# Optimization experiments

Measured on AMD Instinct MI355X. Metric: run time of the kernel, lower is better.

## Reference

```python
import jax, jax.numpy as jnp
import numpy as np

EPS = 1e-5
DIL = 2
PAD = 2  # dilation * (kernel_size - 1) // 2


def _conv(x, w, dil, pad):
    return jax.lax.conv_general_dilated(
        x, w, window_strides=(1, 1), padding=[(pad, pad), (pad, pad)],
        rhs_dilation=(dil, dil), dimension_numbers=('NCHW', 'OIHW', 'NCHW'))


def _bn(x, g, b):
    # BatchNorm2d in training mode: per-channel batch stats over (N,H,W)
    m = x.mean(axis=(0, 2, 3), keepdims=True)
    v = x.var(axis=(0, 2, 3), keepdims=True)
    return (x - m) * jax.lax.rsqrt(v + EPS) * g[None, :, None, None] + b[None, :, None, None]


def _deform_conv(x, offset, w, dil=DIL, pad=PAD):
    # torchvision deform_conv2d v1 (no modulation): offset [B, 2*K, H, W] with
    # channel ordering (dy_0, dx_0, dy_1, dx_1, ...), kernel tap k = ky*3 + kx.
    B, C, H, W = x.shape
    Co = w.shape[0]
    K = 9
    off = offset.reshape(B, K, 2, H, W)
    dy, dx = off[:, :, 0], off[:, :, 1]              # [B,K,H,W]
    kr = jnp.arange(3)
    kyy = (jnp.repeat(kr, 3) * dil - pad).astype(x.dtype)   # [K]
    kxx = (jnp.tile(kr, 3) * dil - pad).astype(x.dtype)     # [K]
    hg = jnp.arange(H, dtype=x.dtype)
    wg = jnp.arange(W, dtype=x.dtype)
    py = hg[None, None, :, None] + kyy[None, :, None, None] + dy   # [B,K,H,W]
    px = wg[None, None, None, :] + kxx[None, :, None, None] + dx   # [B,K,H,W]
    y0 = jnp.floor(py)
    x0 = jnp.floor(px)
    wy = py - y0   # [B,K,H,W]
    wx = px - x0
    y0i = y0.astype(jnp.int32)
    x0i = x0.astype(jnp.int32)
    x_flat = x.reshape(B, C, H * W)

    def corner(yi, xi):
        valid = ((yi >= 0) & (yi < H) & (xi >= 0) & (xi < W)).astype(x.dtype)  # [B,K,H,W]
        idx = jnp.clip(yi, 0, H - 1) * W + jnp.clip(xi, 0, W - 1)
        v = jax.vmap(lambda xb, ib: xb[:, ib])(x_flat, idx.reshape(B, -1))    # [B,C,K*H*W]
        return v.reshape(B, C, K, H, W) * valid[:, None]

    v00 = corner(y0i, x0i)
    v01 = corner(y0i, x0i + 1)
    v10 = corner(y0i + 1, x0i)
    v11 = corner(y0i + 1, x0i + 1)
    wy_ = wy[:, None]   # [B,1,K,H,W]
    wx_ = wx[:, None]
    sampled = (v00 * (1 - wy_) * (1 - wx_) + v01 * (1 - wy_) * wx_
               + v10 * wy_ * (1 - wx_) + v11 * wy_ * wx_)          # [B,C,K,H,W]
    return jnp.einsum('bckhw,ock->bohw', sampled, w.reshape(Co, C, K))


def setup_inputs() -> dict:
    key = jax.random.key(0)
    ks = jax.random.split(key, 4)
    B, C, H, W = 4, 256, 56, 56
    x = jax.random.normal(ks[0], (B, C, H, W), dtype=jnp.float32)
    w_off = jax.random.normal(ks[1], (18, C, 3, 3), dtype=jnp.float32) * 0.01
    b_off = jnp.zeros((18,), dtype=jnp.float32)
    w1 = jax.random.normal(ks[2], (C, C, 3, 3), dtype=jnp.float32) * (1.0 / np.sqrt(9 * C))
    w2 = jax.random.normal(ks[3], (C, C, 3, 3), dtype=jnp.float32) * (1.0 / np.sqrt(9 * C))
    gamma1 = jnp.ones((C,), dtype=jnp.float32)
    beta1 = jnp.zeros((C,), dtype=jnp.float32)
    gamma2 = jnp.ones((C,), dtype=jnp.float32)
    beta2 = jnp.zeros((C,), dtype=jnp.float32)
    return {'x': x, 'w_off': w_off, 'b_off': b_off, 'w1': w1, 'gamma1': gamma1,
            'beta1': beta1, 'w2': w2, 'gamma2': gamma2, 'beta2': beta2}


def reference(x, w_off, b_off, w1, gamma1, beta1, w2, gamma2, beta2):
    offset = _conv(x, w_off, DIL, PAD) + b_off[None, :, None, None]   # [B,18,H,W]
    out = _deform_conv(x, offset, w1)
    out = jax.nn.relu(_bn(out, gamma1, beta1))
    out = _conv(out, w2, 1, 1)
    out = _bn(out, gamma2, beta2)
    return jax.nn.relu(out + x)
```

## Files before the change

kernel.cpp:

```cpp
#include <hip/hip_runtime.h>

typedef __bf16 bf16;
typedef bf16 bf16x4 __attribute__((ext_vector_type(4)));
typedef bf16 bf16x8 __attribute__((ext_vector_type(8)));
typedef float f32x4 __attribute__((ext_vector_type(4)));

#define CH 256
#define HH 56
#define WW 56
#define HW 3136
#define MM 12544
#define KT 2304

__device__ __forceinline__ void gll16(const bf16* g, bf16* l) {
  __builtin_amdgcn_global_load_lds(
      (const __attribute__((address_space(1))) void*)g,
      (__attribute__((address_space(3))) void*)l, 16, 0, 0);
}

__global__ __launch_bounds__(256) void nchw2nhwc_k(const float* __restrict__ x,
                                                   bf16* __restrict__ o) {
  __shared__ float t[32][33];
  const int b = blockIdx.z, hw0 = blockIdx.x * 32, c0 = blockIdx.y * 32;
  const int tid = threadIdx.x;
  {
    const int cl = tid >> 3, hwl = (tid & 7) * 4;
    f32x4 v = *(const f32x4*)&x[(size_t)(b * CH + c0 + cl) * HW + hw0 + hwl];
#pragma unroll
    for (int i = 0; i < 4; ++i) t[cl][hwl + i] = v[i];
  }
  __syncthreads();
  const int hwl = tid >> 3, cl = (tid & 7) * 4;
  bf16x4 ov;
#pragma unroll
  for (int i = 0; i < 4; ++i) ov[i] = (bf16)t[cl + i][hwl];
  *(bf16x4*)&o[(size_t)(b * HW + hw0 + hwl) * CH + c0 + cl] = ov;
}

__global__ void reorder_w_k(const float* __restrict__ in, bf16* __restrict__ out,
                            int Nsrc, int Ntot) {
  const int idx = blockIdx.x * 256 + threadIdx.x;
  if (idx >= Ntot * KT) return;
  const int o = idx / KT, r = idx - o * KT;
  const int k = r >> 8, c = r & 255;
  float v = (o < Nsrc) ? in[(size_t)(o * CH + c) * 9 + k] : 0.f;
  out[idx] = (bf16)v;
}

__global__ __launch_bounds__(256) void build_deform_k(
    const bf16* __restrict__ xn, const float* __restrict__ offb,
    const float* __restrict__ boff, bf16* __restrict__ A1) {
  const int tid = threadIdx.x;
  const int m = blockIdx.x * 32 + (tid >> 3);
  const int l7 = tid & 7;
  const int b = m / HW, hw = m - b * HW;
  const int h = hw / WW, w = hw - h * WW;
  const float* orow = offb + m * 18;
  const bf16* xb = xn + (size_t)b * HW * CH;
  bf16* dst = A1 + (size_t)m * KT;
  for (int tap = 0; tap < 9; ++tap) {
    const int ky = tap / 3, kx = tap - ky * 3;
    const float dy = orow[2 * tap] + boff[2 * tap];
    const float dx = orow[2 * tap + 1] + boff[2 * tap + 1];
    const float py = (float)(h + ky * 2 - 2) + dy;
    const float px = (float)(w + kx * 2 - 2) + dx;
    const float y0f = floorf(py), x0f = floorf(px);
    const int y0 = (int)y0f, x0 = (int)x0f;
    const float wy = py - y0f, wx = px - x0f;
    const float w00 = (1.f - wy) * (1.f - wx), w01 = (1.f - wy) * wx;
    const float w10 = wy * (1.f - wx), w11 = wy * wx;
    const bool vy0 = (unsigned)y0 < HH, vy1 = (unsigned)(y0 + 1) < HH;
    const bool vx0 = (unsigned)x0 < WW, vx1 = (unsigned)(x0 + 1) < WW;
    const bf16* p00 = xb + (long long)(y0 * WW + x0) * CH;
#pragma unroll
    for (int j = 0; j < 4; ++j) {
      const int cc = j * 64 + l7 * 8;
      bf16x8 v00 = {}, v01 = {}, v10 = {}, v11 = {};
      if (vy0 && vx0) v00 = *(const bf16x8*)(p00 + cc);
      if (vy0 && vx1) v01 = *(const bf16x8*)(p00 + CH + cc);
      if (vy1 && vx0) v10 = *(const bf16x8*)(p00 + WW * CH + cc);
      if (vy1 && vx1) v11 = *(const bf16x8*)(p00 + WW * CH + CH + cc);
      bf16x8 o;
#pragma unroll
      for (int i = 0; i < 8; ++i)
        o[i] = (bf16)(w00 * (float)v00[i] + w01 * (float)v01[i] +
                      w10 * (float)v10[i] + w11 * (float)v11[i]);
      *(bf16x8*)(dst + tap * 256 + cc) = o;
    }
  }
}

template <int MODE, int EPI, int SWZ>
__global__ __launch_bounds__(256, 3) void gemm_k(
    const bf16* __restrict__ Asrc, const bf16* __restrict__ Bt,
    const bf16* __restrict__ zp, bf16* __restrict__ outb,
    float* __restrict__ sS, float* __restrict__ sQ,
    float* __restrict__ offout, const int ksteps, const int dil, const int pad) {
  __shared__ __align__(16) bf16 Ab[2][4096];
  __shared__ __align__(16) bf16 Bb[2][4096];
  const int tid = threadIdx.x;
  int n0, m0;
  if (SWZ) {
    const int gid = blockIdx.x;
    const int swz = (gid & 7) * 98 + (gid >> 3);
    n0 = (swz & 3) * 64;
    m0 = (swz >> 2) * 64;
  } else {
    n0 = blockIdx.x * 64;
    m0 = blockIdx.y * 64;
  }
  const int kbase = blockIdx.z * ksteps * 64;
  const int lane = tid & 63, wv = tid >> 6;
  const int wrM = wv >> 1, wcN = wv & 1;
  const int fr = lane & 15, kg = lane >> 4;
  const int srow = tid >> 3, cpos = tid & 7;
  const int sxor = (cpos ^ (srow & 7)) * 8;

  int bb[2], hh[2], wwv[2];
  const bf16* aptr[2];
  if (MODE == 1) {
#pragma unroll
    for (int pa = 0; pa < 2; ++pa) {
      const int m = m0 + pa * 32 + srow;
      bb[pa] = m / HW;
      const int hw = m - bb[pa] * HW;
      hh[pa] = hw / WW;
      wwv[pa] = hw - hh[pa] * WW;
    }
  } else {
#pragma unroll
    for (int pa = 0; pa < 2; ++pa)
      aptr[pa] = Asrc + (size_t)(m0 + pa * 32 + srow) * KT + kbase + sxor;
  }
  const bf16* bptr[2];
#pragma unroll
  for (int pb = 0; pb < 2; ++pb)
    bptr[pb] = Bt + (size_t)(n0 + pb * 32 + srow) * KT + kbase + sxor;

  f32x4 acc[2][2] = {};

  auto STAGE = [&](int kt, int buf) {
    const int kk = kbase + kt * 64;
#pragma unroll
    for (int pa = 0; pa < 2; ++pa) {
      const bf16* as;
      if (MODE == 0) {
        as = aptr[pa] + kt * 64;
      } else {
        const int tap = kk >> 8, coff = kk & 255;
        const int ky = tap / 3, kx = tap - ky * 3;
        const int y = hh[pa] + ky * dil - pad, xx = wwv[pa] + kx * dil - pad;
        const bool ok = ((unsigned)y < HH) && ((unsigned)xx < WW);
        as = ok ? Asrc + ((size_t)(bb[pa] * HW + y * WW + xx) * CH + coff + sxor)
                : zp + sxor;
      }
      gll16(as, &Ab[buf][(pa * 32 + srow) * 64 + cpos * 8]);
    }
#pragma unroll
    for (int pb = 0; pb < 2; ++pb)
      gll16(bptr[pb] + kt * 64, &Bb[buf][(pb * 32 + srow) * 64 + cpos * 8]);
  };

  auto COMPUTE = [&](int buf) {
#pragma unroll
    for (int kh = 0; kh < 2; ++kh) {
      bf16x8 af[2], bv[2];
#pragma unroll
      for (int mf = 0; mf < 2; ++mf) {
        const int row = wrM * 32 + mf * 16 + fr;
        const int g = (kh * 4 + kg) ^ (row & 7);
        af[mf] = *(const bf16x8*)&Ab[buf][row * 64 + g * 8];
      }
#pragma unroll
      for (int nf = 0; nf < 2; ++nf) {
        const int row = wcN * 32 + nf * 16 + fr;
        const int g = (kh * 4 + kg) ^ (row & 7);
        bv[nf] = *(const bf16x8*)&Bb[buf][row * 64 + g * 8];
      }
#pragma unroll
      for (int mf = 0; mf < 2; ++mf)
#pragma unroll
        for (int nf = 0; nf < 2; ++nf)
          acc[mf][nf] = __builtin_amdgcn_mfma_f32_16x16x32_bf16(af[mf], bv[nf],
                                                                acc[mf][nf], 0, 0, 0);
    }
  };

  STAGE(0, 0);
  STAGE(1, 1);
  int buf = 0;
  for (int kt = 0; kt < ksteps; ++kt) {
    if (kt + 1 < ksteps) {
      asm volatile("s_waitcnt vmcnt(4)" ::: "memory");
    } else {
      asm volatile("s_waitcnt vmcnt(0)" ::: "memory");
    }
    __builtin_amdgcn_s_barrier();
    __builtin_amdgcn_sched_barrier(0);
    COMPUTE(buf);
    __builtin_amdgcn_sched_barrier(0);
    __builtin_amdgcn_s_barrier();
    if (kt + 2 < ksteps) STAGE(kt + 2, buf);
    buf ^= 1;
  }

  if (EPI == 1) {
#pragma unroll
    for (int mf = 0; mf < 2; ++mf) {
      const int rr = m0 + wrM * 32 + mf * 16 + kg * 4;
#pragma unroll
      for (int nf = 0; nf < 2; ++nf) {
        const int col = n0 + wcN * 32 + nf * 16 + fr;
#pragma unroll
        for (int r = 0; r < 4; ++r)
          outb[(size_t)(rr + r) * CH + col] = (bf16)acc[mf][nf][r];
      }
    }
    float ps[2], pq[2];
#pragma unroll
    for (int nf = 0; nf < 2; ++nf) {
      float s = 0.f, q = 0.f;
#pragma unroll
      for (int mf = 0; mf < 2; ++mf)
#pragma unroll
        for (int r = 0; r < 4; ++r) {
          const float v = acc[mf][nf][r];
          s += v;
          q += v * v;
        }
      s += __shfl_xor(s, 16);
      s += __shfl_xor(s, 32);
      q += __shfl_xor(q, 16);
      q += __shfl_xor(q, 32);
      ps[nf] = s;
      pq[nf] = q;
    }
    float* red = (float*)&Ab[0][0];
    if (tid < 128) red[tid] = 0.f;
    __syncthreads();
    if (kg == 0) {
#pragma unroll
      for (int nf = 0; nf < 2; ++nf) {
        const int cb = wcN * 32 + nf * 16 + fr;
        atomicAdd(&red[cb], ps[nf]);
        atomicAdd(&red[64 + cb], pq[nf]);
      }
    }
    __syncthreads();
    if (tid < 64) {
      atomicAdd(&sS[n0 + tid], red[tid]);
      atomicAdd(&sQ[n0 + tid], red[64 + tid]);
    }
  } else {
#pragma unroll
    for (int mf = 0; mf < 2; ++mf) {
      const int rr = m0 + wrM * 32 + mf * 16 + kg * 4;
#pragma unroll
      for (int nf = 0; nf < 2; ++nf) {
        const int col = n0 + wcN * 32 + nf * 16 + fr;
        if (col < 18) {
#pragma unroll
          for (int r = 0; r < 4; ++r)
            atomicAdd(&offout[(size_t)(rr + r) * 18 + col], acc[mf][nf][r]);
        }
      }
    }
  }
}

__global__ void affine_k(const float* __restrict__ s, const float* __restrict__ sq,
                         const float* __restrict__ g, const float* __restrict__ be,
                         float* __restrict__ sc, float* __restrict__ bi) {
  const int c = threadIdx.x;
  const float inv = 1.f / (float)MM;
  const float mean = s[c] * inv;
  const float var = sq[c] * inv - mean * mean;
  const float scale = g[c] * rsqrtf(var + 1e-5f);
  sc[c] = scale;
  bi[c] = be[c] - mean * scale;
}

__global__ __launch_bounds__(256) void a1_kb(const bf16* __restrict__ in,
                                             const float* __restrict__ sc,
                                             const float* __restrict__ bi,
                                             bf16* __restrict__ out) {
  const size_t idx = (size_t)(blockIdx.x * 256 + threadIdx.x) * 8;
  const int c0 = (int)(idx & 255);
  bf16x8 v = *(const bf16x8*)&in[idx];
  bf16x8 o;
#pragma unroll
  for (int i = 0; i < 8; ++i) {
    float r = (float)v[i] * sc[c0 + i] + bi[c0 + i];
    o[i] = (bf16)(r > 0.f ? r : 0.f);
  }
  *(bf16x8*)&out[idx] = o;
}

__global__ __launch_bounds__(256) void final_kb(const bf16* __restrict__ o2,
                                                const float* __restrict__ x,
                                                const float* __restrict__ sc,
                                                const float* __restrict__ bi,
                                                float* __restrict__ out) {
  __shared__ float t[32][33];
  const int b = blockIdx.z, hw0 = blockIdx.x * 32, o0 = blockIdx.y * 32;
  const int tid = threadIdx.x;
  {
    const int hwl = tid >> 3, ol = (tid & 7) * 4;
    bf16x4 v = *(const bf16x4*)&o2[(size_t)(b * HW + hw0 + hwl) * CH + o0 + ol];
#pragma unroll
    for (int i = 0; i < 4; ++i) t[ol + i][hwl] = (float)v[i];
  }
  __syncthreads();
  const int ol = tid >> 3, hwl = (tid & 7) * 4;
  const int ch = o0 + ol;
  const float s = sc[ch], bb = bi[ch];
  const size_t xi = (size_t)(b * CH + ch) * HW + hw0 + hwl;
  f32x4 xv = *(const f32x4*)&x[xi];
  f32x4 r;
#pragma unroll
  for (int i = 0; i < 4; ++i) {
    float v = t[ol][hwl + i] * s + bb + xv[i];
    r[i] = v > 0.f ? v : 0.f;
  }
  *(f32x4*)&out[xi] = r;
}

#define WS_XN 0ULL
#define WS_W1T 6422528ULL
#define WS_W2T 7602176ULL
#define WS_WOF 8781824ULL
#define WS_OFFB 9076736ULL
#define WS_A1 9979904ULL
#define WS_O1 67782656ULL
#define WS_ACT 74205184ULL
#define WS_O2 80627712ULL
#define WS_ZP 87050240ULL
#define WS_STAT 87054336ULL
#define WS_SCB 87058432ULL

extern "C" void kernel_launch(void* const* d_in, const int* in_sizes, int n_in,
                              void* d_out, int out_size, void* d_ws, size_t ws_size,
                              hipStream_t stream) {
  const float* x = (const float*)d_in[0];
  const float* w_off = (const float*)d_in[1];
  const float* b_off = (const float*)d_in[2];
  const float* w1 = (const float*)d_in[3];
  const float* g1 = (const float*)d_in[4];
  const float* be1 = (const float*)d_in[5];
  const float* w2 = (const float*)d_in[6];
  const float* g2 = (const float*)d_in[7];
  const float* be2 = (const float*)d_in[8];
  float* out = (float*)d_out;
  char* ws = (char*)d_ws;

  bf16* xn = (bf16*)(ws + WS_XN);
  bf16* w1t = (bf16*)(ws + WS_W1T);
  bf16* w2t = (bf16*)(ws + WS_W2T);
  bf16* wof = (bf16*)(ws + WS_WOF);
  float* offb = (float*)(ws + WS_OFFB);
  bf16* A1 = (bf16*)(ws + WS_A1);
  bf16* o1 = (bf16*)(ws + WS_O1);
  bf16* act = (bf16*)(ws + WS_ACT);
  bf16* o2 = (bf16*)(ws + WS_O2);
  bf16* zp = (bf16*)(ws + WS_ZP);
  float* s1 = (float*)(ws + WS_STAT);
  float* sq1 = (float*)(ws + WS_STAT + 1024);
  float* s2 = (float*)(ws + WS_STAT + 2048);
  float* sq2 = (float*)(ws + WS_STAT + 3072);
  float* sc1 = (float*)(ws + WS_SCB);
  float* bi1 = (float*)(ws + WS_SCB + 1024);
  float* sc2 = (float*)(ws + WS_SCB + 2048);
  float* bi2 = (float*)(ws + WS_SCB + 3072);

  hipMemsetAsync(ws + WS_ZP, 0, 8192, stream);
  hipMemsetAsync(ws + WS_OFFB, 0, 903168, stream);

  nchw2nhwc_k<<<dim3(98, 8, 4), 256, 0, stream>>>(x, xn);
  reorder_w_k<<<2304, 256, 0, stream>>>(w1, w1t, 256, 256);
  reorder_w_k<<<2304, 256, 0, stream>>>(w2, w2t, 256, 256);
  reorder_w_k<<<576, 256, 0, stream>>>(w_off, wof, 18, 64);

  gemm_k<1, 0, 0><<<dim3(1, 196, 4), 256, 0, stream>>>(
      xn, wof, zp, nullptr, nullptr, nullptr, offb, 9, 2, 2);

  build_deform_k<<<392, 256, 0, stream>>>(xn, offb, b_off, A1);

  gemm_k<0, 1, 1><<<dim3(784), 256, 0, stream>>>(A1, w1t, zp, o1, s1, sq1,
                                                 nullptr, 36, 0, 0);
  affine_k<<<1, 256, 0, stream>>>(s1, sq1, g1, be1, sc1, bi1);
  a1_kb<<<1568, 256, 0, stream>>>(o1, sc1, bi1, act);

  gemm_k<1, 1, 1><<<dim3(784), 256, 0, stream>>>(act, w2t, zp, o2, s2, sq2,
                                                 nullptr, 36, 1, 1);
  affine_k<<<1, 256, 0, stream>>>(s2, sq2, g2, be2, sc2, bi2);

  final_kb<<<dim3(98, 8, 4), 256, 0, stream>>>(o2, x, sc2, bi2, out);
}
```

Baseline: 215.9 us.

## Triple-buffer GEMM, merge weight reorders, fold BN affine into consumers

The GEMM kernel moves from double to triple buffering of its LDS stages, and the K-step count and N-tile become template parameters. With TN=32, the offset-conv GEMM loads only 32 weight rows instead of 64. The three weight-reorder launches become one kernel, and the two affine_k launches are removed by computing BN scale and bias inside a1_kb and final_kb. build_deform_k now uses 16 threads per pixel across twice as many blocks. The extra LDS buffer raises shared memory use and could lower occupancy under launch_bounds(256,3), and the fused kernels recompute the BN statistics for every element.

```diff
diff --git a/kernel.cpp b/kernel.cpp
--- a/kernel.cpp
+++ b/kernel.cpp
@@ -16,6 +16,15 @@
   __builtin_amdgcn_global_load_lds(
       (const __attribute__((address_space(1))) void*)g,
       (__attribute__((address_space(3))) void*)l, 16, 0, 0);
+}
+
+template <int N>
+__device__ __forceinline__ void waitvm() {
+  if constexpr (N == 0) asm volatile("s_waitcnt vmcnt(0)" ::: "memory");
+  else if constexpr (N == 3) asm volatile("s_waitcnt vmcnt(3)" ::: "memory");
+  else if constexpr (N == 4) asm volatile("s_waitcnt vmcnt(4)" ::: "memory");
+  else if constexpr (N == 6) asm volatile("s_waitcnt vmcnt(6)" ::: "memory");
+  else if constexpr (N == 8) asm volatile("s_waitcnt vmcnt(8)" ::: "memory");
 }
 
 __global__ __launch_bounds__(256) void nchw2nhwc_k(const float* __restrict__ x,
@@ -37,22 +46,34 @@
   *(bf16x4*)&o[(size_t)(b * HW + hw0 + hwl) * CH + c0 + cl] = ov;
 }
 
-__global__ void reorder_w_k(const float* __restrict__ in, bf16* __restrict__ out,
-                            int Nsrc, int Ntot) {
-  const int idx = blockIdx.x * 256 + threadIdx.x;
-  if (idx >= Ntot * KT) return;
-  const int o = idx / KT, r = idx - o * KT;
-  const int k = r >> 8, c = r & 255;
-  float v = (o < Nsrc) ? in[(size_t)(o * CH + c) * 9 + k] : 0.f;
-  out[idx] = (bf16)v;
+__global__ void reorder_all_k(const float* __restrict__ w1,
+                              const float* __restrict__ w2,
+                              const float* __restrict__ woff,
+                              bf16* __restrict__ w1t, bf16* __restrict__ w2t,
+                              bf16* __restrict__ wof) {
+  const int gid = blockIdx.x;
+  if (gid < 4608) {
+    const int idx = gid * 256 + threadIdx.x;
+    const float* in = (gid < 2304) ? w1 : w2;
+    bf16* out = (gid < 2304) ? w1t : w2t;
+    const int li = (gid < 2304) ? idx : idx - 2304 * 256;
+    const int o = li / KT, r = li - o * KT;
+    const int k = r >> 8, c = r & 255;
+    out[li] = (bf16)in[(size_t)(o * CH + c) * 9 + k];
+  } else {
+    const int li = (gid - 4608) * 256 + threadIdx.x;
+    const int o = li / KT, r = li - o * KT;
+    const int k = r >> 8, c = r & 255;
+    wof[li] = (bf16)((o < 18) ? woff[(size_t)(o * CH + c) * 9 + k] : 0.f);
+  }
 }
 
 __global__ __launch_bounds__(256) void build_deform_k(
     const bf16* __restrict__ xn, const float* __restrict__ offb,
     const float* __restrict__ boff, bf16* __restrict__ A1) {
   const int tid = threadIdx.x;
-  const int m = blockIdx.x * 32 + (tid >> 3);
-  const int l7 = tid & 7;
+  const int m = blockIdx.x * 16 + (tid >> 4);
+  const int l15 = tid & 15;
   const int b = m / HW, hw = m - b * HW;
   const int h = hw / WW, w = hw - h * WW;
   const float* orow = offb + m * 18;
@@ -73,8 +94,8 @@
     const bool vx0 = (unsigned)x0 < WW, vx1 = (unsigned)(x0 + 1) < WW;
     const bf16* p00 = xb + (long long)(y0 * WW + x0) * CH;
 #pragma unroll
-    for (int j = 0; j < 4; ++j) {
-      const int cc = j * 64 + l7 * 8;
+    for (int j = 0; j < 2; ++j) {
+      const int cc = j * 128 + l15 * 8;
       bf16x8 v00 = {}, v01 = {}, v10 = {}, v11 = {};
       if (vy0 && vx0) v00 = *(const bf16x8*)(p00 + cc);
       if (vy0 && vx1) v01 = *(const bf16x8*)(p00 + CH + cc);
@@ -90,14 +111,17 @@
   }
 }
 
-template <int MODE, int EPI, int SWZ>
+template <int MODE, int EPI, int SWZ, int TN, int KS>
 __global__ __launch_bounds__(256, 3) void gemm_k(
     const bf16* __restrict__ Asrc, const bf16* __restrict__ Bt,
     const bf16* __restrict__ zp, bf16* __restrict__ outb,
     float* __restrict__ sS, float* __restrict__ sQ,
-    float* __restrict__ offout, const int ksteps, const int dil, const int pad) {
-  __shared__ __align__(16) bf16 Ab[2][4096];
-  __shared__ __align__(16) bf16 Bb[2][4096];
+    float* __restrict__ offout, const int dil, const int pad) {
+  constexpr int PB = TN / 32;
+  constexpr int NF = TN / 32;
+  constexpr int SL = 2 + PB;
+  __shared__ __align__(16) bf16 Ab[3][4096];
+  __shared__ __align__(16) bf16 Bb[3][TN * 64];
   const int tid = threadIdx.x;
   int n0, m0;
   if (SWZ) {
@@ -106,10 +130,10 @@
     n0 = (swz & 3) * 64;
     m0 = (swz >> 2) * 64;
   } else {
-    n0 = blockIdx.x * 64;
+    n0 = blockIdx.x * TN;
     m0 = blockIdx.y * 64;
   }
-  const int kbase = blockIdx.z * ksteps * 64;
+  const int kbase = blockIdx.z * KS * 64;
   const int lane = tid & 63, wv = tid >> 6;
   const int wrM = wv >> 1, wcN = wv & 1;
   const int fr = lane & 15, kg = lane >> 4;
@@ -132,12 +156,12 @@
     for (int pa = 0; pa < 2; ++pa)
       aptr[pa] = Asrc + (size_t)(m0 + pa * 32 + srow) * KT + kbase + sxor;
   }
-  const bf16* bptr[2];
-#pragma unroll
-  for (int pb = 0; pb < 2; ++pb)
+  const bf16* bptr[PB];
+#pragma unroll
+  for (int pb = 0; pb < PB; ++pb)
     bptr[pb] = Bt + (size_t)(n0 + pb * 32 + srow) * KT + kbase + sxor;
 
-  f32x4 acc[2][2] = {};
+  f32x4 acc[2][NF] = {};
 
   auto STAGE = [&](int kt, int buf) {
     const int kk = kbase + kt * 64;
@@ -157,14 +181,14 @@
       gll16(as, &Ab[buf][(pa * 32 + srow) * 64 + cpos * 8]);
     }
 #pragma unroll
-    for (int pb = 0; pb < 2; ++pb)
+    for (int pb = 0; pb < PB; ++pb)
       gll16(bptr[pb] + kt * 64, &Bb[buf][(pb * 32 + srow) * 64 + cpos * 8]);
   };
 
   auto COMPUTE = [&](int buf) {
 #pragma unroll
     for (int kh = 0; kh < 2; ++kh) {
-      bf16x8 af[2], bv[2];
+      bf16x8 af[2], bv[NF];
 #pragma unroll
       for (int mf = 0; mf < 2; ++mf) {
         const int row = wrM * 32 + mf * 16 + fr;
@@ -172,15 +196,15 @@
         af[mf] = *(const bf16x8*)&Ab[buf][row * 64 + g * 8];
       }
 #pragma unroll
-      for (int nf = 0; nf < 2; ++nf) {
-        const int row = wcN * 32 + nf * 16 + fr;
+      for (int nf = 0; nf < NF; ++nf) {
+        const int row = wcN * (NF * 16) + nf * 16 + fr;
         const int g = (kh * 4 + kg) ^ (row & 7);
         bv[nf] = *(const bf16x8*)&Bb[buf][row * 64 + g * 8];
       }
 #pragma unroll
       for (int mf = 0; mf < 2; ++mf)
 #pragma unroll
-        for (int nf = 0; nf < 2; ++nf)
+        for (int nf = 0; nf < NF; ++nf)
           acc[mf][nf] = __builtin_amdgcn_mfma_f32_16x16x32_bf16(af[mf], bv[nf],
                                                                 acc[mf][nf], 0, 0, 0);
     }
@@ -188,37 +212,36 @@
 
   STAGE(0, 0);
   STAGE(1, 1);
-  int buf = 0;
-  for (int kt = 0; kt < ksteps; ++kt) {
-    if (kt + 1 < ksteps) {
-      asm volatile("s_waitcnt vmcnt(4)" ::: "memory");
-    } else {
-      asm volatile("s_waitcnt vmcnt(0)" ::: "memory");
-    }
+  STAGE(2, 2);
+#pragma unroll 3
+  for (int kt = 0; kt < KS; ++kt) {
+    const int buf = kt % 3;
+    if (kt < KS - 2) waitvm<2 * SL>();
+    else if (kt == KS - 2) waitvm<SL>();
+    else waitvm<0>();
     __builtin_amdgcn_s_barrier();
     __builtin_amdgcn_sched_barrier(0);
     COMPUTE(buf);
     __builtin_amdgcn_sched_barrier(0);
     __builtin_amdgcn_s_barrier();
-    if (kt + 2 < ksteps) STAGE(kt + 2, buf);
-    buf ^= 1;
-  }
-
-  if (EPI == 1) {
+    if (kt + 3 < KS) STAGE(kt + 3, buf);
+  }
+
+  if constexpr (EPI == 1) {
 #pragma unroll
     for (int mf = 0; mf < 2; ++mf) {
       const int rr = m0 + wrM * 32 + mf * 16 + kg * 4;
 #pragma unroll
-      for (int nf = 0; nf < 2; ++nf) {
-        const int col = n0 + wcN * 32 + nf * 16 + fr;
+      for (int nf = 0; nf < NF; ++nf) {
+        const int col = n0 + wcN * (NF * 16) + nf * 16 + fr;
 #pragma unroll
         for (int r = 0; r < 4; ++r)
           outb[(size_t)(rr + r) * CH + col] = (bf16)acc[mf][nf][r];
       }
     }
-    float ps[2], pq[2];
-#pragma unroll
-    for (int nf = 0; nf < 2; ++nf) {
+    float ps[NF], pq[NF];
+#pragma unroll
+    for (int nf = 0; nf < NF; ++nf) {
       float s = 0.f, q = 0.f;
 #pragma unroll
       for (int mf = 0; mf < 2; ++mf)
@@ -240,8 +263,8 @@
     __syncthreads();
     if (kg == 0) {
 #pragma unroll
-      for (int nf = 0; nf < 2; ++nf) {
-        const int cb = wcN * 32 + nf * 16 + fr;
+      for (int nf = 0; nf < NF; ++nf) {
+        const int cb = wcN * (NF * 16) + nf * 16 + fr;
         atomicAdd(&red[cb], ps[nf]);
         atomicAdd(&red[64 + cb], pq[nf]);
       }
@@ -256,8 +279,8 @@
     for (int mf = 0; mf < 2; ++mf) {
       const int rr = m0 + wrM * 32 + mf * 16 + kg * 4;
 #pragma unroll
-      for (int nf = 0; nf < 2; ++nf) {
-        const int col = n0 + wcN * 32 + nf * 16 + fr;
+      for (int nf = 0; nf < NF; ++nf) {
+        const int col = n0 + wcN * (NF * 16) + nf * 16 + fr;
         if (col < 18) {
 #pragma unroll
           for (int r = 0; r < 4; ++r)
@@ -268,29 +291,25 @@
   }
 }
 
-__global__ void affine_k(const float* __restrict__ s, const float* __restrict__ sq,
-                         const float* __restrict__ g, const float* __restrict__ be,
-                         float* __restrict__ sc, float* __restrict__ bi) {
-  const int c = threadIdx.x;
-  const float inv = 1.f / (float)MM;
-  const float mean = s[c] * inv;
-  const float var = sq[c] * inv - mean * mean;
-  const float scale = g[c] * rsqrtf(var + 1e-5f);
-  sc[c] = scale;
-  bi[c] = be[c] - mean * scale;
-}
-
 __global__ __launch_bounds__(256) void a1_kb(const bf16* __restrict__ in,
-                                             const float* __restrict__ sc,
-                                             const float* __restrict__ bi,
+                                             const float* __restrict__ s,
+                                             const float* __restrict__ sq,
+                                             const float* __restrict__ g,
+                                             const float* __restrict__ be,
                                              bf16* __restrict__ out) {
   const size_t idx = (size_t)(blockIdx.x * 256 + threadIdx.x) * 8;
   const int c0 = (int)(idx & 255);
+  const float inv = 1.f / (float)MM;
   bf16x8 v = *(const bf16x8*)&in[idx];
   bf16x8 o;
 #pragma unroll
   for (int i = 0; i < 8; ++i) {
-    float r = (float)v[i] * sc[c0 + i] + bi[c0 + i];
+    const int c = c0 + i;
+    const float mean = s[c] * inv;
+    const float var = sq[c] * inv - mean * mean;
+    const float sc = g[c] * rsqrtf(var + 1e-5f);
+    const float bi = be[c] - mean * sc;
+    float r = (float)v[i] * sc + bi;
     o[i] = (bf16)(r > 0.f ? r : 0.f);
   }
   *(bf16x8*)&out[idx] = o;
@@ -298,8 +317,10 @@
 
 __global__ __launch_bounds__(256) void final_kb(const bf16* __restrict__ o2,
                                                 const float* __restrict__ x,
-                                                const float* __restrict__ sc,
-                                                const float* __restrict__ bi,
+                                                const float* __restrict__ s,
+                                                const float* __restrict__ sq,
+                                                const float* __restrict__ g,
+                                                const float* __restrict__ be,
                                                 float* __restrict__ out) {
   __shared__ float t[32][33];
   const int b = blockIdx.z, hw0 = blockIdx.x * 32, o0 = blockIdx.y * 32;
@@ -313,13 +334,17 @@
   __syncthreads();
   const int ol = tid >> 3, hwl = (tid & 7) * 4;
   const int ch = o0 + ol;
-  const float s = sc[ch], bb = bi[ch];
+  const float inv = 1.f / (float)MM;
+  const float mean = s[ch] * inv;
+  const float var = sq[ch] * inv - mean * mean;
+  const float sc = g[ch] * rsqrtf(var + 1e-5f);
+  const float bb = be[ch] - mean * sc;
   const size_t xi = (size_t)(b * CH + ch) * HW + hw0 + hwl;
   f32x4 xv = *(const f32x4*)&x[xi];
   f32x4 r;
 #pragma unroll
   for (int i = 0; i < 4; ++i) {
-    float v = t[ol][hwl + i] * s + bb + xv[i];
+    float v = t[ol][hwl + i] * sc + bb + xv[i];
     r[i] = v > 0.f ? v : 0.f;
   }
   *(f32x4*)&out[xi] = r;
@@ -336,7 +361,6 @@
 #define WS_O2 80627712ULL
 #define WS_ZP 87050240ULL
 #define WS_STAT 87054336ULL
-#define WS_SCB 87058432ULL
 
 extern "C" void kernel_launch(void* const* d_in, const int* in_sizes, int n_in,
                               void* d_out, int out_size, void* d_ws, size_t ws_size,
@@ -367,32 +391,24 @@
   float* sq1 = (float*)(ws + WS_STAT + 1024);
   float* s2 = (float*)(ws + WS_STAT + 2048);
   float* sq2 = (float*)(ws + WS_STAT + 3072);
-  float* sc1 = (float*)(ws + WS_SCB);
-  float* bi1 = (float*)(ws + WS_SCB + 1024);
-  float* sc2 = (float*)(ws + WS_SCB + 2048);
-  float* bi2 = (float*)(ws + WS_SCB + 3072);
 
   hipMemsetAsync(ws + WS_ZP, 0, 8192, stream);
   hipMemsetAsync(ws + WS_OFFB, 0, 903168, stream);
 
   nchw2nhwc_k<<<dim3(98, 8, 4), 256, 0, stream>>>(x, xn);
-  reorder_w_k<<<2304, 256, 0, stream>>>(w1, w1t, 256, 256);
-  reorder_w_k<<<2304, 256, 0, stream>>>(w2, w2t, 256, 256);
-  reorder_w_k<<<576, 256, 0, stream>>>(w_off, wof, 18, 64);
-
-  gemm_k<1, 0, 0><<<dim3(1, 196, 4), 256, 0, stream>>>(
-      xn, wof, zp, nullptr, nullptr, nullptr, offb, 9, 2, 2);
-
-  build_deform_k<<<392, 256, 0, stream>>>(xn, offb, b_off, A1);
-
-  gemm_k<0, 1, 1><<<dim3(784), 256, 0, stream>>>(A1, w1t, zp, o1, s1, sq1,
-                                                 nullptr, 36, 0, 0);
-  affine_k<<<1, 256, 0, stream>>>(s1, sq1, g1, be1, sc1, bi1);
-  a1_kb<<<1568, 256, 0, stream>>>(o1, sc1, bi1, act);
-
-  gemm_k<1, 1, 1><<<dim3(784), 256, 0, stream>>>(act, w2t, zp, o2, s2, sq2,
-                                                 nullptr, 36, 1, 1);
-  affine_k<<<1, 256, 0, stream>>>(s2, sq2, g2, be2, sc2, bi2);
-
-  final_kb<<<dim3(98, 8, 4), 256, 0, stream>>>(o2, x, sc2, bi2, out);
-}
+  reorder_all_k<<<5184, 256, 0, stream>>>(w1, w2, w_off, w1t, w2t, wof);
+
+  gemm_k<1, 0, 0, 32, 9><<<dim3(1, 196, 4), 256, 0, stream>>>(
+      xn, wof, zp, nullptr, nullptr, nullptr, offb, 2, 2);
+
+  build_deform_k<<<784, 256, 0, stream>>>(xn, offb, b_off, A1);
+
+  gemm_k<0, 1, 1, 64, 36><<<dim3(784), 256, 0, stream>>>(
+      A1, w1t, zp, o1, s1, sq1, nullptr, 0, 0);
+  a1_kb<<<1568, 256, 0, stream>>>(o1, s1, sq1, g1, be1, act);
+
+  gemm_k<1, 1, 1, 64, 36><<<dim3(784), 256, 0, stream>>>(
+      act, w2t, zp, o2, s2, sq2, nullptr, 1, 1);
+
+  final_kb<<<dim3(98, 8, 4), 256, 0, stream>>>(o2, x, s2, sq2, g2, be2, out);
+}
```

Measured after the change: 237.1 us. 1.1x slower.
